# Kernel tuning notes

Measured on AMD Instinct MI355X. Metric: run time of the kernel, lower is better.

Reference implementation:

```python
import jax, jax.numpy as jnp
import numpy as np

N_NODES = 100000
N_EDGES = 3200000
D_IN, D_HID, D_OUT = 512, 16, 64


def setup_inputs() -> dict:
    key = jax.random.key(0)
    ks = jax.random.split(key, 7)
    x = jax.random.normal(ks[0], (N_NODES, D_IN), jnp.float32)
    edge_index = jax.random.randint(ks[1], (2, N_EDGES), 0, N_NODES, dtype=jnp.int32)
    edge_weight = jax.random.uniform(ks[2], (N_EDGES,), jnp.float32)
    W1 = jax.random.normal(ks[3], (D_IN, D_HID), jnp.float32) * (1.0 / np.sqrt(D_IN))
    b1 = jnp.zeros((D_HID,), jnp.float32)
    W2 = jax.random.normal(ks[4], (D_HID, D_OUT), jnp.float32) * (1.0 / np.sqrt(D_HID))
    b2 = jnp.zeros((D_OUT,), jnp.float32)
    return {"x": x, "edge_index": edge_index, "edge_weight": edge_weight,
            "W1": W1, "b1": b1, "W2": W2, "b2": b2}


def reference(x, edge_index, edge_weight, W1, b1, W2, b2):
    N = x.shape[0]
    loop = jnp.arange(N, dtype=edge_index.dtype)
    # GCNConv(normalize=True): add self-loops (weight 1), symmetric normalization
    src = jnp.concatenate([edge_index[0], loop])
    dst = jnp.concatenate([edge_index[1], loop])
    w = jnp.concatenate([edge_weight, jnp.ones((N,), x.dtype)])
    deg = jax.ops.segment_sum(w, dst, num_segments=N)
    dinv = jnp.where(deg > 0, jax.lax.rsqrt(deg), 0.0)
    norm = dinv[src] * w * dinv[dst]  # [E+N]

    def gcn_conv(h, W, b):
        h = h @ W  # transform first (thin GEMM), then aggregate
        msg = h[src] * norm[:, None]  # gather + scale
        return jax.ops.segment_sum(msg, dst, num_segments=N) + b  # scatter-add

    h = jax.nn.relu(gcn_conv(x, W1, b1))
    # F.dropout is identity in eval mode
    out = gcn_conv(h, W2, b2)
    return jax.nn.log_softmax(out, axis=1)
```

## Files before the change

kernel.cpp:

```cpp
#include <hip/hip_runtime.h>
#include <hip/hip_bf16.h>


#define D_IN 512
#define D_HID 16
#define D_OUT 64
#define BDIM 128
#define BSHIFT 7
#define NBLK0 512

__global__ __launch_bounds__(256) void p0_count(const int* __restrict__ dst,
                                                int* __restrict__ bcnt,
                                                int NBUCK, int E, int chunk) {
    extern __shared__ int hist[];
    int k = blockIdx.x;
    for (int i = threadIdx.x; i < NBUCK; i += 256) hist[i] = 0;
    __syncthreads();
    int beg = k * chunk, end = min(beg + chunk, E);
    for (int e = beg + threadIdx.x; e < end; e += 256)
        atomicAdd(&hist[dst[e] >> BSHIFT], 1);
    __syncthreads();
    for (int i = threadIdx.x; i < NBUCK; i += 256)
        bcnt[(size_t)k * NBUCK + i] = hist[i];
}

__global__ __launch_bounds__(256) void p_scan1(int* __restrict__ bcnt,
                                               int* __restrict__ btot, int NBUCK) {
    __shared__ int s[256];
    int b = blockIdx.x, t = threadIdx.x;
    int v0 = bcnt[(size_t)(2 * t) * NBUCK + b];
    int v1 = bcnt[(size_t)(2 * t + 1) * NBUCK + b];
    int pair = v0 + v1;
    s[t] = pair;
    __syncthreads();
    for (int off = 1; off < 256; off <<= 1) {
        int v = (t >= off) ? s[t - off] : 0;
        __syncthreads();
        s[t] += v;
        __syncthreads();
    }
    int ex = s[t] - pair;
    bcnt[(size_t)(2 * t) * NBUCK + b] = ex;
    bcnt[(size_t)(2 * t + 1) * NBUCK + b] = ex + v0;
    if (t == 255) btot[b] = s[255];
}

__global__ __launch_bounds__(1024) void p_scan2(const int* __restrict__ btot,
                                                int* __restrict__ bbase,
                                                int NBUCK, int E) {
    __shared__ int s[1024];
    int t = threadIdx.x;
    int v = (t < NBUCK) ? btot[t] : 0;
    s[t] = v;
    __syncthreads();
    for (int off = 1; off < 1024; off <<= 1) {
        int u = (t >= off) ? s[t - off] : 0;
        __syncthreads();
        s[t] += u;
        __syncthreads();
    }
    if (t < NBUCK) bbase[t] = s[t] - v;
    if (t == 0) bbase[NBUCK] = E;
}

__global__ __launch_bounds__(256) void p1_scatter(const int* __restrict__ src,
                                                  const int* __restrict__ dst,
                                                  const float* __restrict__ w,
                                                  const int* __restrict__ bcnt,
                                                  const int* __restrict__ bbase,
                                                  float2* __restrict__ tmp,
                                                  int NBUCK, int E, int chunk) {
    extern __shared__ int cur[];
    int k = blockIdx.x;
    for (int i = threadIdx.x; i < NBUCK; i += 256)
        cur[i] = bbase[i] + bcnt[(size_t)k * NBUCK + i];
    __syncthreads();
    int beg = k * chunk, end = min(beg + chunk, E);
    for (int e = beg + threadIdx.x; e < end; e += 256) {
        int d = dst[e];
        int b = d >> BSHIFT;
        int pos = atomicAdd(&cur[b], 1);
        tmp[pos] = make_float2(__int_as_float(((d & (BDIM - 1)) << 24) | src[e]), w[e]);
    }
}

__global__ __launch_bounds__(256) void p4a_count(const float2* __restrict__ tmp,
                                                 const int* __restrict__ bbase,
                                                 int* __restrict__ row_start,
                                                 float* __restrict__ dinv,
                                                 int NBUCK, int N, int E) {
    __shared__ int cnt[BDIM];
    __shared__ float wdeg[BDIM];
    __shared__ int pre[BDIM];
    int b = blockIdx.x;
    if (threadIdx.x < BDIM) { cnt[threadIdx.x] = 0; wdeg[threadIdx.x] = 0.0f; }
    __syncthreads();
    int beg = bbase[b], end = bbase[b + 1];
    for (int e = beg + threadIdx.x; e < end; e += 256) {
        float2 p = tmp[e];
        int dl = ((unsigned)__float_as_int(p.x)) >> 24;
        atomicAdd(&cnt[dl], 1);
        atomicAdd(&wdeg[dl], p.y);
    }
    __syncthreads();
    if (threadIdx.x < BDIM) pre[threadIdx.x] = cnt[threadIdx.x];
    __syncthreads();
    for (int off = 1; off < BDIM; off <<= 1) {
        int add = 0;
        if (threadIdx.x < BDIM && threadIdx.x >= off) add = pre[threadIdx.x - off];
        __syncthreads();
        if (threadIdx.x < BDIM) pre[threadIdx.x] += add;
        __syncthreads();
    }
    if (threadIdx.x < BDIM) {
        int node = (b << BSHIFT) + threadIdx.x;
        if (node < N) {
            row_start[node] = beg + pre[threadIdx.x] - cnt[threadIdx.x];
            dinv[node] = __frsqrt_rn(1.0f + wdeg[threadIdx.x]);
        }
    }
    if (b == NBUCK - 1 && threadIdx.x == 0) row_start[N] = E;
}

__global__ __launch_bounds__(256) void p4b_scatter(const float2* __restrict__ tmp,
                                                   const int* __restrict__ bbase,
                                                   const int* __restrict__ row_start,
                                                   const float* __restrict__ dinv,
                                                   float2* __restrict__ sorted, int N) {
    __shared__ int cur[BDIM];
    __shared__ float dl_dinv[BDIM];
    int b = blockIdx.x;
    if (threadIdx.x < BDIM) {
        int node = (b << BSHIFT) + threadIdx.x;
        cur[threadIdx.x] = (node < N) ? row_start[node] : 0;
        dl_dinv[threadIdx.x] = (node < N) ? dinv[node] : 0.0f;
    }
    __syncthreads();
    int beg = bbase[b], end = bbase[b + 1];
    for (int e = beg + threadIdx.x; e < end; e += 256) {
        float2 p = tmp[e];
        unsigned u = (unsigned)__float_as_int(p.x);
        int dl = u >> 24;
        int s = (int)(u & 0xFFFFFFu);
        int pos = atomicAdd(&cur[dl], 1);
        float nw = p.y * dinv[s] * dl_dinv[dl];
        sorted[pos] = make_float2(__int_as_float(s), nw);
    }
}

__global__ __launch_bounds__(256) void gemm1_kernel(const float* __restrict__ x,
                                                    const float* __restrict__ W1,
                                                    float* __restrict__ t, int N) {
    __shared__ float w1t[16 * 520];
    for (int idx = threadIdx.x; idx < D_IN * D_HID; idx += 256) {
        int k = idx >> 4, j = idx & 15;
        w1t[j * 520 + k] = W1[idx];
    }
    __syncthreads();

    const int wave = threadIdx.x >> 6;
    const int lane = threadIdx.x & 63;
    const int g = lane >> 4;
    const int s = lane & 15;

    for (int base = blockIdx.x * 16; base < N; base += gridDim.x * 16) {
        int row = base + wave * 4 + g;
        if (row < N) {
            const float4* xr = (const float4*)(x + (size_t)row * D_IN);
            float4 xv[8];
#pragma unroll
            for (int i = 0; i < 8; ++i) xv[i] = xr[s + 16 * i];
            float acc[16];
#pragma unroll
            for (int j = 0; j < 16; ++j) acc[j] = 0.0f;
#pragma unroll
            for (int i = 0; i < 8; ++i) {
                int kb = 4 * s + 64 * i;
#pragma unroll
                for (int j = 0; j < 16; ++j) {
                    const float4 wv = *(const float4*)&w1t[j * 520 + kb];
                    acc[j] += xv[i].x * wv.x + xv[i].y * wv.y + xv[i].z * wv.z + xv[i].w * wv.w;
                }
            }
#pragma unroll
            for (int j = 0; j < 16; ++j) {
#pragma unroll
                for (int m = 1; m < 16; m <<= 1) acc[j] += __shfl_xor(acc[j], m, 64);
            }
            float v = acc[0];
#pragma unroll
            for (int j = 1; j < 16; ++j) v = (s == j) ? acc[j] : v;
            t[(size_t)row * 16 + s] = v;
        }
    }
}

template <int LAYER>
__global__ __launch_bounds__(256) void agg_kernel(const float2* __restrict__ sorted,
                                                  const int* __restrict__ row_start,
                                                  const float* __restrict__ feat,
                                                  const float* __restrict__ dinv,
                                                  const float* __restrict__ b1,
                                                  const float* __restrict__ W2,
                                                  const float* __restrict__ b2,
                                                  float* __restrict__ outp, int N) {
    __shared__ float w2s[16 * 64];
    __shared__ float b2s[64];
    if (LAYER == 2) {
        for (int idx = threadIdx.x; idx < 16 * 64; idx += 256) w2s[idx] = W2[idx];
        if (threadIdx.x < 64) b2s[threadIdx.x] = b2[threadIdx.x];
        __syncthreads();
    }
    int node = blockIdx.x * 4 + (threadIdx.x >> 6);
    if (node >= N) return;
    int lane = threadIdx.x & 63;
    int j = lane & 15, k = lane >> 4;
    int beg = row_start[node], end = row_start[node + 1];
    float acc = 0.0f;
    int i0 = beg;
    if ((i0 & 1) && i0 < end) {
        if (k == 0) {
            float2 p = sorted[i0];
            acc += p.y * feat[(size_t)__float_as_int(p.x) * 16 + j];
        }
        ++i0;
    }
    for (int e = i0 + 2 * k; e + 1 < end; e += 8) {
        float4 q = *(const float4*)(sorted + e);
        int s0 = __float_as_int(q.x);
        int s1 = __float_as_int(q.z);
        acc += q.y * feat[(size_t)s0 * 16 + j];
        acc += q.w * feat[(size_t)s1 * 16 + j];
    }
    if ((end > i0) && ((end - i0) & 1) && k == 0) {
        float2 p = sorted[end - 1];
        acc += p.y * feat[(size_t)__float_as_int(p.x) * 16 + j];
    }
    acc += __shfl_xor(acc, 16, 64);
    acc += __shfl_xor(acc, 32, 64);
    float dn = dinv[node];
    float r = acc + dn * dn * feat[(size_t)node * 16 + j];
    if (LAYER == 1) {
        r = fmaxf(r + b1[j], 0.0f);
        if (lane < 16) outp[(size_t)node * 16 + j] = r;
    } else {
        float z = b2s[lane];
#pragma unroll
        for (int j2 = 0; j2 < 16; ++j2)
            z += __shfl(r, j2, 64) * w2s[j2 * 64 + lane];
        float m = z;
#pragma unroll
        for (int off = 32; off; off >>= 1) m = fmaxf(m, __shfl_xor(m, off, 64));
        float ez = __expf(z - m);
        float ssum = ez;
#pragma unroll
        for (int off = 32; off; off >>= 1) ssum += __shfl_xor(ssum, off, 64);
        outp[(size_t)node * 64 + lane] = z - m - __logf(ssum);
    }
}

extern "C" void kernel_launch(void* const* d_in, const int* in_sizes, int n_in,
                              void* d_out, int out_size, void* d_ws, size_t ws_size,
                              hipStream_t stream) {
    const float* x  = (const float*)d_in[0];
    const int*   ei = (const int*)d_in[1];
    const float* ew = (const float*)d_in[2];
    const float* W1 = (const float*)d_in[3];
    const float* b1 = (const float*)d_in[4];
    const float* W2 = (const float*)d_in[5];
    const float* b2 = (const float*)d_in[6];
    float* out = (float*)d_out;

    const int N = in_sizes[0] / D_IN;
    const int E = in_sizes[2];
    const int* srcI = ei;
    const int* dstI = ei + E;

    const int NBUCK = (N + BDIM - 1) >> BSHIFT;
    const int chunk = (E + NBLK0 - 1) / NBLK0;

    float* ws = (float*)d_ws;
    size_t o = 0;
    float* dinv      = ws + o;         o += (size_t)N;             o = (o + 3) & ~(size_t)3;
    int*   row_start = (int*)(ws + o); o += (size_t)N + 2;         o = (o + 3) & ~(size_t)3;
    int*   bbase     = (int*)(ws + o); o += (size_t)NBUCK + 1;     o = (o + 3) & ~(size_t)3;
    int*   btot      = (int*)(ws + o); o += (size_t)NBUCK;         o = (o + 3) & ~(size_t)3;
    int*   bcnt      = (int*)(ws + o); o += (size_t)NBLK0 * NBUCK; o = (o + 3) & ~(size_t)3;
    float* tmpR      = ws + o;
    size_t tmpsz = (size_t)2 * E; if ((size_t)32 * N > tmpsz) tmpsz = (size_t)32 * N;
    o += tmpsz;                                                    o = (o + 3) & ~(size_t)3;
    float2* sorted   = (float2*)(ws + o);

    float2* tmp = (float2*)tmpR;
    float*  t   = tmpR;
    float*  h1  = tmpR + (size_t)16 * N;

    p0_count<<<NBLK0, 256, NBUCK * sizeof(int), stream>>>(dstI, bcnt, NBUCK, E, chunk);
    p_scan1<<<NBUCK, 256, 0, stream>>>(bcnt, btot, NBUCK);
    p_scan2<<<1, 1024, 0, stream>>>(btot, bbase, NBUCK, E);
    p1_scatter<<<NBLK0, 256, NBUCK * sizeof(int), stream>>>(srcI, dstI, ew, bcnt, bbase,
                                                            tmp, NBUCK, E, chunk);
    p4a_count<<<NBUCK, 256, 0, stream>>>(tmp, bbase, row_start, dinv, NBUCK, N, E);
    p4b_scatter<<<NBUCK, 256, 0, stream>>>(tmp, bbase, row_start, dinv, sorted, N);

    gemm1_kernel<<<1024, 256, 0, stream>>>(x, W1, t, N);

    agg_kernel<1><<<(N + 3) / 4, 256, 0, stream>>>(sorted, row_start, t, dinv,
                                                   b1, W2, b2, h1, N);
    agg_kernel<2><<<(N + 3) / 4, 256, 0, stream>>>(sorted, row_start, h1, dinv,
                                                   b1, W2, b2, out, N);
}
```

Before: 631.7 us.

## Vectorize edge loads in bucket sort passes and use float4 gathers in aggregation

The count and scatter passes now read dst/src/weight with int4/float4 loads, four edges per thread, and the chunk size is rounded to a multiple of four so those loads stay aligned. The per-bucket count and scatter kernels read tmp two pairs at a time as float4. The aggregation kernel assigns each lane four features through float4 gathers, so one wave covers 16 edges per step instead of 4, with a wider shuffle reduction. The gemm1 grid is also doubled. The aim is fewer memory instructions and more loads in flight; the cost is extra tail handling and more registers.

```diff
diff --git a/kernel.cpp b/kernel.cpp
--- a/kernel.cpp
+++ b/kernel.cpp
@@ -17,8 +17,16 @@
     for (int i = threadIdx.x; i < NBUCK; i += 256) hist[i] = 0;
     __syncthreads();
     int beg = k * chunk, end = min(beg + chunk, E);
-    for (int e = beg + threadIdx.x; e < end; e += 256)
-        atomicAdd(&hist[dst[e] >> BSHIFT], 1);
+    int e = beg + threadIdx.x * 4;
+    for (; e + 3 < end; e += 1024) {
+        int4 d4 = *(const int4*)(dst + e);
+        atomicAdd(&hist[d4.x >> BSHIFT], 1);
+        atomicAdd(&hist[d4.y >> BSHIFT], 1);
+        atomicAdd(&hist[d4.z >> BSHIFT], 1);
+        atomicAdd(&hist[d4.w >> BSHIFT], 1);
+    }
+    for (int q = e; q < min(e + 4, end); ++q)
+        atomicAdd(&hist[dst[q] >> BSHIFT], 1);
     __syncthreads();
     for (int i = threadIdx.x; i < NBUCK; i += 256)
         bcnt[(size_t)k * NBUCK + i] = hist[i];
@@ -76,11 +84,24 @@
         cur[i] = bbase[i] + bcnt[(size_t)k * NBUCK + i];
     __syncthreads();
     int beg = k * chunk, end = min(beg + chunk, E);
-    for (int e = beg + threadIdx.x; e < end; e += 256) {
-        int d = dst[e];
-        int b = d >> BSHIFT;
-        int pos = atomicAdd(&cur[b], 1);
-        tmp[pos] = make_float2(__int_as_float(((d & (BDIM - 1)) << 24) | src[e]), w[e]);
+    int e = beg + threadIdx.x * 4;
+    for (; e + 3 < end; e += 1024) {
+        int4   s4 = *(const int4*)(src + e);
+        int4   d4 = *(const int4*)(dst + e);
+        float4 w4 = *(const float4*)(w + e);
+        int p0 = atomicAdd(&cur[d4.x >> BSHIFT], 1);
+        tmp[p0] = make_float2(__int_as_float(((d4.x & (BDIM - 1)) << 24) | s4.x), w4.x);
+        int p1 = atomicAdd(&cur[d4.y >> BSHIFT], 1);
+        tmp[p1] = make_float2(__int_as_float(((d4.y & (BDIM - 1)) << 24) | s4.y), w4.y);
+        int p2 = atomicAdd(&cur[d4.z >> BSHIFT], 1);
+        tmp[p2] = make_float2(__int_as_float(((d4.z & (BDIM - 1)) << 24) | s4.z), w4.z);
+        int p3 = atomicAdd(&cur[d4.w >> BSHIFT], 1);
+        tmp[p3] = make_float2(__int_as_float(((d4.w & (BDIM - 1)) << 24) | s4.w), w4.w);
+    }
+    for (int q = e; q < min(e + 4, end); ++q) {
+        int d = dst[q];
+        int pos = atomicAdd(&cur[d >> BSHIFT], 1);
+        tmp[pos] = make_float2(__int_as_float(((d & (BDIM - 1)) << 24) | src[q]), w[q]);
     }
 }
 
@@ -96,8 +117,24 @@
     if (threadIdx.x < BDIM) { cnt[threadIdx.x] = 0; wdeg[threadIdx.x] = 0.0f; }
     __syncthreads();
     int beg = bbase[b], end = bbase[b + 1];
-    for (int e = beg + threadIdx.x; e < end; e += 256) {
-        float2 p = tmp[e];
+    int vbeg = beg + (beg & 1);
+    if ((beg & 1) && beg < end && threadIdx.x == 0) {
+        float2 p = tmp[beg];
+        int dl = ((unsigned)__float_as_int(p.x)) >> 24;
+        atomicAdd(&cnt[dl], 1);
+        atomicAdd(&wdeg[dl], p.y);
+    }
+    for (int e = vbeg + 2 * threadIdx.x; e + 1 < end; e += 512) {
+        float4 q = *(const float4*)(tmp + e);
+        int dl0 = ((unsigned)__float_as_int(q.x)) >> 24;
+        int dl1 = ((unsigned)__float_as_int(q.z)) >> 24;
+        atomicAdd(&cnt[dl0], 1);
+        atomicAdd(&wdeg[dl0], q.y);
+        atomicAdd(&cnt[dl1], 1);
+        atomicAdd(&wdeg[dl1], q.w);
+    }
+    if ((end > vbeg) && ((end - vbeg) & 1) && threadIdx.x == 0) {
+        float2 p = tmp[end - 1];
         int dl = ((unsigned)__float_as_int(p.x)) >> 24;
         atomicAdd(&cnt[dl], 1);
         atomicAdd(&wdeg[dl], p.y);
@@ -137,14 +174,31 @@
     }
     __syncthreads();
     int beg = bbase[b], end = bbase[b + 1];
-    for (int e = beg + threadIdx.x; e < end; e += 256) {
-        float2 p = tmp[e];
+    int vbeg = beg + (beg & 1);
+    if ((beg & 1) && beg < end && threadIdx.x == 0) {
+        float2 p = tmp[beg];
         unsigned u = (unsigned)__float_as_int(p.x);
-        int dl = u >> 24;
-        int s = (int)(u & 0xFFFFFFu);
+        int dl = u >> 24, s = (int)(u & 0xFFFFFFu);
         int pos = atomicAdd(&cur[dl], 1);
-        float nw = p.y * dinv[s] * dl_dinv[dl];
-        sorted[pos] = make_float2(__int_as_float(s), nw);
+        sorted[pos] = make_float2(__int_as_float(s), p.y * dinv[s] * dl_dinv[dl]);
+    }
+    for (int e = vbeg + 2 * threadIdx.x; e + 1 < end; e += 512) {
+        float4 q = *(const float4*)(tmp + e);
+        unsigned u0 = (unsigned)__float_as_int(q.x);
+        unsigned u1 = (unsigned)__float_as_int(q.z);
+        int dl0 = u0 >> 24, s0 = (int)(u0 & 0xFFFFFFu);
+        int dl1 = u1 >> 24, s1 = (int)(u1 & 0xFFFFFFu);
+        int pos0 = atomicAdd(&cur[dl0], 1);
+        sorted[pos0] = make_float2(__int_as_float(s0), q.y * dinv[s0] * dl_dinv[dl0]);
+        int pos1 = atomicAdd(&cur[dl1], 1);
+        sorted[pos1] = make_float2(__int_as_float(s1), q.w * dinv[s1] * dl_dinv[dl1]);
+    }
+    if ((end > vbeg) && ((end - vbeg) & 1) && threadIdx.x == 0) {
+        float2 p = tmp[end - 1];
+        unsigned u = (unsigned)__float_as_int(p.x);
+        int dl = u >> 24, s = (int)(u & 0xFFFFFFu);
+        int pos = atomicAdd(&cur[dl], 1);
+        sorted[pos] = make_float2(__int_as_float(s), p.y * dinv[s] * dl_dinv[dl]);
     }
 }
 
@@ -213,41 +267,69 @@
     }
     int node = blockIdx.x * 4 + (threadIdx.x >> 6);
     if (node >= N) return;
-    int lane = threadIdx.x & 63;
-    int j = lane & 15, k = lane >> 4;
+    const int lane = threadIdx.x & 63;
+    const int jq = lane & 3;
+    const int k = lane >> 2;
+    const float4* feat4 = (const float4*)feat;
     int beg = row_start[node], end = row_start[node + 1];
-    float acc = 0.0f;
+    float ax = 0.f, ay = 0.f, az = 0.f, aw = 0.f;
     int i0 = beg;
     if ((i0 & 1) && i0 < end) {
         if (k == 0) {
             float2 p = sorted[i0];
-            acc += p.y * feat[(size_t)__float_as_int(p.x) * 16 + j];
+            float4 f = feat4[(size_t)__float_as_int(p.x) * 4 + jq];
+            ax += p.y * f.x; ay += p.y * f.y; az += p.y * f.z; aw += p.y * f.w;
         }
         ++i0;
     }
-    for (int e = i0 + 2 * k; e + 1 < end; e += 8) {
+    for (int e = i0 + 2 * k; e + 1 < end; e += 32) {
         float4 q = *(const float4*)(sorted + e);
         int s0 = __float_as_int(q.x);
         int s1 = __float_as_int(q.z);
-        acc += q.y * feat[(size_t)s0 * 16 + j];
-        acc += q.w * feat[(size_t)s1 * 16 + j];
+        float4 f0 = feat4[(size_t)s0 * 4 + jq];
+        float4 f1 = feat4[(size_t)s1 * 4 + jq];
+        ax += q.y * f0.x + q.w * f1.x;
+        ay += q.y * f0.y + q.w * f1.y;
+        az += q.y * f0.z + q.w * f1.z;
+        aw += q.y * f0.w + q.w * f1.w;
     }
     if ((end > i0) && ((end - i0) & 1) && k == 0) {
         float2 p = sorted[end - 1];
-        acc += p.y * feat[(size_t)__float_as_int(p.x) * 16 + j];
-    }
-    acc += __shfl_xor(acc, 16, 64);
-    acc += __shfl_xor(acc, 32, 64);
+        float4 f = feat4[(size_t)__float_as_int(p.x) * 4 + jq];
+        ax += p.y * f.x; ay += p.y * f.y; az += p.y * f.z; aw += p.y * f.w;
+    }
+#pragma unroll
+    for (int m = 4; m < 64; m <<= 1) {
+        ax += __shfl_xor(ax, m, 64);
+        ay += __shfl_xor(ay, m, 64);
+        az += __shfl_xor(az, m, 64);
+        aw += __shfl_xor(aw, m, 64);
+    }
     float dn = dinv[node];
-    float r = acc + dn * dn * feat[(size_t)node * 16 + j];
+    float dnn = dn * dn;
+    float4 fs = feat4[(size_t)node * 4 + jq];
+    float rx = ax + dnn * fs.x;
+    float ry = ay + dnn * fs.y;
+    float rz = az + dnn * fs.z;
+    float rw = aw + dnn * fs.w;
     if (LAYER == 1) {
-        r = fmaxf(r + b1[j], 0.0f);
-        if (lane < 16) outp[(size_t)node * 16 + j] = r;
+        float4 bq = ((const float4*)b1)[jq];
+        rx = fmaxf(rx + bq.x, 0.0f);
+        ry = fmaxf(ry + bq.y, 0.0f);
+        rz = fmaxf(rz + bq.z, 0.0f);
+        rw = fmaxf(rw + bq.w, 0.0f);
+        if (k == 0) ((float4*)outp)[(size_t)node * 4 + jq] = make_float4(rx, ry, rz, rw);
     } else {
         float z = b2s[lane];
 #pragma unroll
-        for (int j2 = 0; j2 < 16; ++j2)
-            z += __shfl(r, j2, 64) * w2s[j2 * 64 + lane];
+        for (int q2 = 0; q2 < 4; ++q2) {
+            float bx = __shfl(rx, q2, 64);
+            float by = __shfl(ry, q2, 64);
+            float bz = __shfl(rz, q2, 64);
+            float bw = __shfl(rw, q2, 64);
+            z += bx * w2s[(4 * q2 + 0) * 64 + lane] + by * w2s[(4 * q2 + 1) * 64 + lane]
+               + bz * w2s[(4 * q2 + 2) * 64 + lane] + bw * w2s[(4 * q2 + 3) * 64 + lane];
+        }
         float m = z;
 #pragma unroll
         for (int off = 32; off; off >>= 1) m = fmaxf(m, __shfl_xor(m, off, 64));
@@ -277,7 +359,7 @@
     const int* dstI = ei + E;
 
     const int NBUCK = (N + BDIM - 1) >> BSHIFT;
-    const int chunk = (E + NBLK0 - 1) / NBLK0;
+    const int chunk = (((E + NBLK0 - 1) / NBLK0) + 3) & ~3;
 
     float* ws = (float*)d_ws;
     size_t o = 0;
@@ -303,7 +385,7 @@
     p4a_count<<<NBUCK, 256, 0, stream>>>(tmp, bbase, row_start, dinv, NBUCK, N, E);
     p4b_scatter<<<NBUCK, 256, 0, stream>>>(tmp, bbase, row_start, dinv, sorted, N);
 
-    gemm1_kernel<<<1024, 256, 0, stream>>>(x, W1, t, N);
+    gemm1_kernel<<<2048, 256, 0, stream>>>(x, W1, t, N);
 
     agg_kernel<1><<<(N + 3) / 4, 256, 0, stream>>>(sorted, row_start, t, dinv,
                                                    b1, W2, b2, h1, N);
```

New measurement: 575.1 us. 1.1x faster.
